# Kernel optimization log

Hardware: AMD Instinct MI355X
Metric: run time of the kernel (lower is better)

## Reference

```python
import jax, jax.numpy as jnp
import numpy as np

N, IN_DIM, OUT_DIM, H = 8192, 128, 128, 2
HD = OUT_DIM // H
NEG_SLOPE = 0.2


def setup_inputs() -> dict:
    key = jax.random.key(0)
    k1, k2, k3, k4, k5 = jax.random.split(key, 5)
    x = jax.random.normal(k1, (N, IN_DIM), dtype=jnp.float32)
    adj = jax.random.randint(k2, (N, N), 0, 2).astype(jnp.float32)
    W = jax.random.normal(k3, (IN_DIM, OUT_DIM), dtype=jnp.float32) / np.sqrt(IN_DIM)
    a_src = jax.random.normal(k4, (H, HD), dtype=jnp.float32) * 0.01
    a_dst = jax.random.normal(k5, (H, HD), dtype=jnp.float32) * 0.01
    return {"x": x, "adj": adj, "W": W, "a_src": a_src, "a_dst": a_dst}


def reference(x, adj, W, a_src, a_dst):
    # h: (N, H, HD)
    h = (x @ W).reshape(N, H, HD)
    # per-node additive score halves: (N, H)
    e_src = jnp.einsum('nhd,hd->nh', h, a_src)
    e_dst = jnp.einsum('nhd,hd->nh', h, a_dst)
    # attn logits: (N_i, N_j, H); torch code adds e_src[i] + e_dst[j]
    logits = jax.nn.leaky_relu(e_src[:, None, :] + e_dst[None, :, :], NEG_SLOPE)
    logits = jnp.where(adj[:, :, None] > 0, logits, -jnp.inf)
    # softmax over neighbor axis j (dim=1), matching F.softmax(attn, dim=1)
    attn = jax.nn.softmax(logits, axis=1)
    # dropout omitted (eval mode)
    out = jnp.einsum('ijh,jhd->ihd', attn, h).reshape(N, OUT_DIM)
    return out
```

## Files before the change

### kernel.cpp

```cpp
#include <hip/hip_runtime.h>
#include <hip/hip_bf16.h>

#define N 8192
#define IND 128
#define OUTD 128
#define JC 8
#define JLEN 1024
#define OSTEPS 8
#define NW64 (N / 64)

typedef float f32x4 __attribute__((ext_vector_type(4)));
typedef short s16x8 __attribute__((ext_vector_type(8)));
typedef _Float16 f16;
typedef _Float16 f16x4 __attribute__((ext_vector_type(4)));

static __device__ inline unsigned short f2bf(float f) {
    union { float f; unsigned u; } v; v.f = f;
    unsigned u = v.u + 0x7fffu + ((v.u >> 16) & 1u);
    return (unsigned short)(u >> 16);
}
static __device__ inline float bf2f(unsigned short b) {
    union { unsigned u; float f; } v; v.u = ((unsigned)b) << 16;
    return v.f;
}
static __device__ __forceinline__ unsigned pkbf(float a, float b) {
    __hip_bfloat162 t = __float22bfloat162_rn(make_float2(a, b));
    unsigned u;
    __builtin_memcpy(&u, &t, 4);
    return u;
}

__global__ __launch_bounds__(256) void k0_pack(const float* __restrict__ adj,
                                               unsigned long long* __restrict__ bits) {
    const int row = blockIdx.x;
    const int wave = threadIdx.x >> 6, lane = threadIdx.x & 63;
    const float* src = adj + (size_t)row * N + wave * 2048;
    unsigned long long acc = 0;
#pragma unroll 8
    for (int t = 0; t < 32; ++t) {
        float v = src[t * 64 + lane];
        unsigned long long b = __ballot(v != 0.0f);
        if (lane == t) acc = b;
    }
    if (lane < 32)
        bits[(size_t)row * NW64 + wave * 32 + lane] = acc;
}

__global__ __launch_bounds__(256) void k1_xw(const float* __restrict__ x,
                                             const float* __restrict__ W,
                                             unsigned short* __restrict__ hT) {
    __shared__ unsigned short Wl[128 * 130];
    const int tid = threadIdx.x;
    {
        int k = tid >> 1, n0 = (tid & 1) * 64;
        const float4* src = (const float4*)(W + k * 128 + n0);
#pragma unroll
        for (int v = 0; v < 16; ++v) {
            float4 f = src[v];
            int base = k * 130 + n0 + v * 4;
            Wl[base + 0] = f2bf(f.x);
            Wl[base + 1] = f2bf(f.y);
            Wl[base + 2] = f2bf(f.z);
            Wl[base + 3] = f2bf(f.w);
        }
    }
    __syncthreads();
    const int wave = tid >> 6, lane = tid & 63;
    const int m = lane & 15, quad = lane >> 4;
    const int ibase = blockIdx.x * 64 + wave * 16;
    const int irow = ibase + m;

    f32x4 acc[8];
#pragma unroll
    for (int t = 0; t < 8; ++t) acc[t] = (f32x4){0.f, 0.f, 0.f, 0.f};

#pragma unroll
    for (int ks = 0; ks < 4; ++ks) {
        const int k0 = ks * 32 + quad * 8;
        const float4* xp = (const float4*)(x + (size_t)irow * 128 + k0);
        float4 xa = xp[0], xb = xp[1];
        s16x8 afrag;
        afrag[0] = (short)f2bf(xa.x); afrag[1] = (short)f2bf(xa.y);
        afrag[2] = (short)f2bf(xa.z); afrag[3] = (short)f2bf(xa.w);
        afrag[4] = (short)f2bf(xb.x); afrag[5] = (short)f2bf(xb.y);
        afrag[6] = (short)f2bf(xb.z); afrag[7] = (short)f2bf(xb.w);
#pragma unroll
        for (int nt = 0; nt < 8; ++nt) {
            const int n = nt * 16 + m;
            s16x8 bfrag;
#pragma unroll
            for (int j = 0; j < 8; ++j)
                bfrag[j] = (short)Wl[(k0 + j) * 130 + n];
            acc[nt] = __builtin_amdgcn_mfma_f32_16x16x32_bf16(afrag, bfrag, acc[nt], 0, 0, 0);
        }
    }
#pragma unroll
    for (int nt = 0; nt < 8; ++nt) {
        const int c = nt * 16 + m;
        const int i0 = ibase + quad * 4;
        ushort4 pk;
        pk.x = f2bf(acc[nt][0]); pk.y = f2bf(acc[nt][1]);
        pk.z = f2bf(acc[nt][2]); pk.w = f2bf(acc[nt][3]);
        *(ushort4*)(hT + (size_t)c * N + i0) = pk;
    }
}

__global__ __launch_bounds__(256) void k2_e(const unsigned short* __restrict__ hT,
                                            const float* __restrict__ a_src,
                                            const float* __restrict__ a_dst,
                                            float* __restrict__ As, float* __restrict__ Cs,
                                            float4* __restrict__ BD) {
    const int i = blockIdx.x * 256 + threadIdx.x;
    float es0 = 0.f, ed0 = 0.f, es1 = 0.f, ed1 = 0.f;
#pragma unroll 8
    for (int c = 0; c < 128; ++c) {
        float v = bf2f(hT[(size_t)c * N + i]);
        float as = a_src[c], ad = a_dst[c];
        if (c < 64) { es0 += v * as; ed0 += v * ad; }
        else        { es1 += v * as; ed1 += v * ad; }
    }
    As[i]     = __expf(es0);
    As[N + i] = __expf(es1);
    Cs[i]     = __expf(0.2f * es0);
    Cs[N + i] = __expf(0.2f * es1);
    float4 bd;
    bd.x = __expf(ed0); bd.y = __expf(0.2f * ed0);
    bd.z = __expf(ed1); bd.w = __expf(0.2f * ed1);
    BD[i] = bd;
}

__global__ __launch_bounds__(256, 4) void k3_main(const unsigned long long* __restrict__ bits,
                                                  const unsigned short* __restrict__ hT,
                                                  const float* __restrict__ As,
                                                  const float* __restrict__ Cs,
                                                  const float4* __restrict__ BD,
                                                  f16* __restrict__ Up,
                                                  float* __restrict__ Lp) {
    __shared__ float4 BDl[JLEN + JLEN / 8];
    const int tid = threadIdx.x;
    const int wave = tid >> 6, lane = tid & 63;
    const int m = lane & 15, quad = lane >> 4;
    const int ibase = blockIdx.x * 64 + wave * 16;
    const int irow = ibase + m;
    const int jc = blockIdx.y;
    const int j0 = jc * JLEN;

    for (int t = tid; t < JLEN; t += 256) BDl[t + (t >> 3)] = BD[j0 + t];

    const float A0 = As[irow], C0 = Cs[irow];
    const float A1 = As[N + irow], C1 = Cs[N + irow];

    f32x4 acc[2][4];
#pragma unroll
    for (int h = 0; h < 2; ++h)
#pragma unroll
        for (int nt = 0; nt < 4; ++nt) acc[h][nt] = (f32x4){0.f, 0.f, 0.f, 0.f};
    f32x4 accS[2];
    accS[0] = (f32x4){0.f, 0.f, 0.f, 0.f};
    accS[1] = (f32x4){0.f, 0.f, 0.f, 0.f};

    s16x8 ones;
#pragma unroll
    for (int t = 0; t < 8; ++t) ones[t] = (short)0x3F80;

    const unsigned long long* mrow = bits + (size_t)irow * NW64 + (j0 >> 6);
    const int shbase = quad * 8;
    __syncthreads();

#pragma unroll 2
    for (int os = 0; os < OSTEPS; ++os) {
        const unsigned long long mk0 = mrow[os * 2];
        const unsigned long long mk1 = mrow[os * 2 + 1];
#pragma unroll
        for (int kc = 0; kc < 4; ++kc) {
            const int jq = j0 + os * 128 + kc * 32 + quad * 8;
            s16x8 h0[4], h1[4];
#pragma unroll
            for (int nt = 0; nt < 4; ++nt) {
                h0[nt] = *(const s16x8*)(hT + (size_t)(nt * 16 + m) * N + jq);
                h1[nt] = *(const s16x8*)(hT + (size_t)(nt * 16 + m + 64) * N + jq);
            }
            const unsigned long long mk = (kc < 2) ? mk0 : mk1;
            const unsigned mbyte = (unsigned)(mk >> ((kc & 1) * 32 + shbase)) & 0xffu;

            const int bb = os * 128 + kc * 32 + quad * 8;
            const int bidx = bb + (bb >> 3);
            float pv0[8], pv1[8];
#pragma unroll
            for (int jj = 0; jj < 8; ++jj) {
                float4 bd = BDl[bidx + jj];
                float w0 = fmaxf(A0 * bd.x, C0 * bd.y);
                float w1 = fmaxf(A1 * bd.z, C1 * bd.w);
                bool on = (mbyte >> jj) & 1u;
                pv0[jj] = on ? w0 : 0.0f;
                pv1[jj] = on ? w1 : 0.0f;
            }
            unsigned pu0[4], pu1[4];
#pragma unroll
            for (int t = 0; t < 4; ++t) {
                pu0[t] = pkbf(pv0[t * 2], pv0[t * 2 + 1]);
                pu1[t] = pkbf(pv1[t * 2], pv1[t * 2 + 1]);
            }
            s16x8 p0, p1;
            __builtin_memcpy(&p0, pu0, 16);
            __builtin_memcpy(&p1, pu1, 16);

#pragma unroll
            for (int nt = 0; nt < 4; ++nt) {
                acc[0][nt] = __builtin_amdgcn_mfma_f32_16x16x32_bf16(p0, h0[nt], acc[0][nt], 0, 0, 0);
                acc[1][nt] = __builtin_amdgcn_mfma_f32_16x16x32_bf16(p1, h1[nt], acc[1][nt], 0, 0, 0);
            }
            accS[0] = __builtin_amdgcn_mfma_f32_16x16x32_bf16(p0, ones, accS[0], 0, 0, 0);
            accS[1] = __builtin_amdgcn_mfma_f32_16x16x32_bf16(p1, ones, accS[1], 0, 0, 0);
        }
    }

    f16* Ub = Up + (size_t)jc * N * 128;
#pragma unroll
    for (int h = 0; h < 2; ++h)
#pragma unroll
        for (int nt = 0; nt < 4; ++nt) {
            const int c = h * 64 + nt * 16 + m;
            const int ib = ibase + quad * 4;
#pragma unroll
            for (int r = 0; r < 4; ++r)
                Ub[(size_t)(ib + r) * 128 + c] = (f16)acc[h][nt][r];
        }
    if (m == 0) {
#pragma unroll
        for (int h = 0; h < 2; ++h)
#pragma unroll
            for (int r = 0; r < 4; ++r)
                Lp[((size_t)jc * 2 + h) * N + ibase + quad * 4 + r] = accS[h][r];
    }
}

__global__ __launch_bounds__(256) void k4_reduce(const f16* __restrict__ Up,
                                                 const float* __restrict__ Lp,
                                                 float* __restrict__ out) {
    const int base = (blockIdx.x * 256 + threadIdx.x) * 4;
    const int i = base >> 7, c = base & 127, h = c >> 6;
    float su0 = 0.f, su1 = 0.f, su2 = 0.f, su3 = 0.f, sl = 0.f;
#pragma unroll
    for (int jcc = 0; jcc < JC; ++jcc) {
        f16x4 u = *(const f16x4*)(Up + (size_t)jcc * N * 128 + base);
        su0 += (float)u[0]; su1 += (float)u[1];
        su2 += (float)u[2]; su3 += (float)u[3];
        sl += Lp[((size_t)jcc * 2 + h) * N + i];
    }
    float inv = 1.0f / sl;
    float4 o; o.x = su0 * inv; o.y = su1 * inv; o.z = su2 * inv; o.w = su3 * inv;
    *(float4*)(out + base) = o;
}

extern "C" void kernel_launch(void* const* d_in, const int* in_sizes, int n_in,
                              void* d_out, int out_size, void* d_ws, size_t ws_size,
                              hipStream_t stream) {
    const float* x     = (const float*)d_in[0];
    const float* adj   = (const float*)d_in[1];
    const float* W     = (const float*)d_in[2];
    const float* a_src = (const float*)d_in[3];
    const float* a_dst = (const float*)d_in[4];
    float* out = (float*)d_out;
    char* ws = (char*)d_ws;

    size_t off = 0;
    unsigned short* hT = (unsigned short*)(ws + off); off += (size_t)128 * N * 2;
    float* As = (float*)(ws + off); off += (size_t)2 * N * 4;
    float* Cs = (float*)(ws + off); off += (size_t)2 * N * 4;
    float4* BD = (float4*)(ws + off); off += (size_t)N * 16;
    unsigned long long* bits = (unsigned long long*)(ws + off); off += (size_t)N * NW64 * 8;

    f16* Up = (f16*)(ws + off);
    float* Lp = (float*)(ws + off + (size_t)JC * N * 128 * 2);

    k0_pack<<<N, 256, 0, stream>>>(adj, bits);
    k1_xw<<<N / 64, 256, 0, stream>>>(x, W, hT);
    k2_e<<<N / 256, 256, 0, stream>>>(hT, a_src, a_dst, As, Cs, BD);
    dim3 g3(N / 64, JC);
    k3_main<<<g3, 256, 0, stream>>>(bits, hT, As, Cs, BD, Up, Lp);
    k4_reduce<<<(N * 128) / (256 * 4), 256, 0, stream>>>(Up, Lp, out);
}
```

Before: 515.0 us.

## Double-buffer hT loads in main loop and reduce split-K partials with atomics

```diff
diff --git a/kernel.cpp b/kernel.cpp
--- a/kernel.cpp
+++ b/kernel.cpp
@@ -6,13 +6,11 @@
 #define OUTD 128
 #define JC 8
 #define JLEN 1024
-#define OSTEPS 8
+#define TSTEPS 32
 #define NW64 (N / 64)
 
 typedef float f32x4 __attribute__((ext_vector_type(4)));
 typedef short s16x8 __attribute__((ext_vector_type(8)));
-typedef _Float16 f16;
-typedef _Float16 f16x4 __attribute__((ext_vector_type(4)));
 
 static __device__ inline unsigned short f2bf(float f) {
     union { float f; unsigned u; } v; v.f = f;
@@ -36,7 +34,7 @@
     const int wave = threadIdx.x >> 6, lane = threadIdx.x & 63;
     const float* src = adj + (size_t)row * N + wave * 2048;
     unsigned long long acc = 0;
-#pragma unroll 8
+#pragma unroll
     for (int t = 0; t < 32; ++t) {
         float v = src[t * 64 + lane];
         unsigned long long b = __ballot(v != 0.0f);
@@ -129,14 +127,15 @@
     BD[i] = bd;
 }
 
-__global__ __launch_bounds__(256, 4) void k3_main(const unsigned long long* __restrict__ bits,
+__global__ __launch_bounds__(256, 3) void k3_main(const unsigned long long* __restrict__ bits,
                                                   const unsigned short* __restrict__ hT,
                                                   const float* __restrict__ As,
                                                   const float* __restrict__ Cs,
                                                   const float4* __restrict__ BD,
-                                                  f16* __restrict__ Up,
+                                                  float* __restrict__ Up,
                                                   float* __restrict__ Lp) {
-    __shared__ float4 BDl[JLEN + JLEN / 8];
+    __shared__ float smem[4 * 16 * 129];
+    float4* BDl = (float4*)smem;
     const int tid = threadIdx.x;
     const int wave = tid >> 6, lane = tid & 63;
     const int m = lane & 15, quad = lane >> 4;
@@ -164,92 +163,99 @@
     for (int t = 0; t < 8; ++t) ones[t] = (short)0x3F80;
 
     const unsigned long long* mrow = bits + (size_t)irow * NW64 + (j0 >> 6);
-    const int shbase = quad * 8;
     __syncthreads();
 
-#pragma unroll 2
-    for (int os = 0; os < OSTEPS; ++os) {
-        const unsigned long long mk0 = mrow[os * 2];
-        const unsigned long long mk1 = mrow[os * 2 + 1];
-#pragma unroll
-        for (int kc = 0; kc < 4; ++kc) {
-            const int jq = j0 + os * 128 + kc * 32 + quad * 8;
-            s16x8 h0[4], h1[4];
-#pragma unroll
-            for (int nt = 0; nt < 4; ++nt) {
-                h0[nt] = *(const s16x8*)(hT + (size_t)(nt * 16 + m) * N + jq);
-                h1[nt] = *(const s16x8*)(hT + (size_t)(nt * 16 + m + 64) * N + jq);
-            }
-            const unsigned long long mk = (kc < 2) ? mk0 : mk1;
-            const unsigned mbyte = (unsigned)(mk >> ((kc & 1) * 32 + shbase)) & 0xffu;
-
-            const int bb = os * 128 + kc * 32 + quad * 8;
-            const int bidx = bb + (bb >> 3);
-            float pv0[8], pv1[8];
-#pragma unroll
-            for (int jj = 0; jj < 8; ++jj) {
-                float4 bd = BDl[bidx + jj];
-                float w0 = fmaxf(A0 * bd.x, C0 * bd.y);
-                float w1 = fmaxf(A1 * bd.z, C1 * bd.w);
-                bool on = (mbyte >> jj) & 1u;
-                pv0[jj] = on ? w0 : 0.0f;
-                pv1[jj] = on ? w1 : 0.0f;
-            }
-            unsigned pu0[4], pu1[4];
-#pragma unroll
-            for (int t = 0; t < 4; ++t) {
-                pu0[t] = pkbf(pv0[t * 2], pv0[t * 2 + 1]);
-                pu1[t] = pkbf(pv1[t * 2], pv1[t * 2 + 1]);
-            }
-            s16x8 p0, p1;
-            __builtin_memcpy(&p0, pu0, 16);
-            __builtin_memcpy(&p1, pu1, 16);
-
-#pragma unroll
-            for (int nt = 0; nt < 4; ++nt) {
-                acc[0][nt] = __builtin_amdgcn_mfma_f32_16x16x32_bf16(p0, h0[nt], acc[0][nt], 0, 0, 0);
-                acc[1][nt] = __builtin_amdgcn_mfma_f32_16x16x32_bf16(p1, h1[nt], acc[1][nt], 0, 0, 0);
-            }
-            accS[0] = __builtin_amdgcn_mfma_f32_16x16x32_bf16(p0, ones, accS[0], 0, 0, 0);
-            accS[1] = __builtin_amdgcn_mfma_f32_16x16x32_bf16(p1, ones, accS[1], 0, 0, 0);
-        }
-    }
-
-    f16* Ub = Up + (size_t)jc * N * 128;
+    s16x8 hb[2][8];
+    {
+        const int jq0 = j0 + quad * 8;
+#pragma unroll
+        for (int nt = 0; nt < 4; ++nt) {
+            hb[0][nt]     = *(const s16x8*)(hT + (size_t)(nt * 16 + m) * N + jq0);
+            hb[0][4 + nt] = *(const s16x8*)(hT + (size_t)(nt * 16 + m + 64) * N + jq0);
+        }
+    }
+
+#pragma unroll 4
+    for (int t = 0; t < TSTEPS; ++t) {
+        const int cur = t & 1, nxt = cur ^ 1;
+        const int tn = (t < TSTEPS - 1) ? t + 1 : t;
+        const int jqn = j0 + tn * 32 + quad * 8;
+#pragma unroll
+        for (int nt = 0; nt < 4; ++nt) {
+            hb[nxt][nt]     = *(const s16x8*)(hT + (size_t)(nt * 16 + m) * N + jqn);
+            hb[nxt][4 + nt] = *(const s16x8*)(hT + (size_t)(nt * 16 + m + 64) * N + jqn);
+        }
+
+        const unsigned long long mk = mrow[t >> 1];
+        const unsigned mbyte = (unsigned)(mk >> ((t & 1) * 32 + quad * 8)) & 0xffu;
+
+        const int bb = t * 32 + quad * 8;
+        const int bidx = bb + (bb >> 3);
+        float pv0[8], pv1[8];
+#pragma unroll
+        for (int jj = 0; jj < 8; ++jj) {
+            float4 bd = BDl[bidx + jj];
+            float w0 = fmaxf(A0 * bd.x, C0 * bd.y);
+            float w1 = fmaxf(A1 * bd.z, C1 * bd.w);
+            bool on = (mbyte >> jj) & 1u;
+            pv0[jj] = on ? w0 : 0.0f;
+            pv1[jj] = on ? w1 : 0.0f;
+        }
+        unsigned pu0[4], pu1[4];
+#pragma unroll
+        for (int q = 0; q < 4; ++q) {
+            pu0[q] = pkbf(pv0[q * 2], pv0[q * 2 + 1]);
+            pu1[q] = pkbf(pv1[q * 2], pv1[q * 2 + 1]);
+        }
+        s16x8 p0, p1;
+        __builtin_memcpy(&p0, pu0, 16);
+        __builtin_memcpy(&p1, pu1, 16);
+
+#pragma unroll
+        for (int nt = 0; nt < 4; ++nt) {
+            acc[0][nt] = __builtin_amdgcn_mfma_f32_16x16x32_bf16(p0, hb[cur][nt], acc[0][nt], 0, 0, 0);
+            acc[1][nt] = __builtin_amdgcn_mfma_f32_16x16x32_bf16(p1, hb[cur][4 + nt], acc[1][nt], 0, 0, 0);
+        }
+        accS[0] = __builtin_amdgcn_mfma_f32_16x16x32_bf16(p0, ones, accS[0], 0, 0, 0);
+        accS[1] = __builtin_amdgcn_mfma_f32_16x16x32_bf16(p1, ones, accS[1], 0, 0, 0);
+    }
+
+    __syncthreads();
+    float* sm = smem + wave * 16 * 129;
 #pragma unroll
     for (int h = 0; h < 2; ++h)
 #pragma unroll
         for (int nt = 0; nt < 4; ++nt) {
             const int c = h * 64 + nt * 16 + m;
-            const int ib = ibase + quad * 4;
 #pragma unroll
             for (int r = 0; r < 4; ++r)
-                Ub[(size_t)(ib + r) * 128 + c] = (f16)acc[h][nt][r];
-        }
+                sm[(quad * 4 + r) * 129 + c] = acc[h][nt][r];
+        }
+#pragma unroll
+    for (int r16 = 0; r16 < 16; ++r16) {
+        float v0 = sm[r16 * 129 + lane];
+        float v1 = sm[r16 * 129 + 64 + lane];
+        const size_t o = (size_t)(ibase + r16) * 128 + lane;
+        atomicAdd(&Up[o], v0);
+        atomicAdd(&Up[o + 64], v1);
+    }
     if (m == 0) {
 #pragma unroll
         for (int h = 0; h < 2; ++h)
 #pragma unroll
             for (int r = 0; r < 4; ++r)
-                Lp[((size_t)jc * 2 + h) * N + ibase + quad * 4 + r] = accS[h][r];
-    }
-}
-
-__global__ __launch_bounds__(256) void k4_reduce(const f16* __restrict__ Up,
-                                                 const float* __restrict__ Lp,
-                                                 float* __restrict__ out) {
+                atomicAdd(&Lp[h * N + ibase + quad * 4 + r], accS[h][r]);
+    }
+}
+
+__global__ __launch_bounds__(256) void k4_norm(const float* __restrict__ Up,
+                                               const float* __restrict__ Lp,
+                                               float* __restrict__ out) {
     const int base = (blockIdx.x * 256 + threadIdx.x) * 4;
-    const int i = base >> 7, c = base & 127, h = c >> 6;
-    float su0 = 0.f, su1 = 0.f, su2 = 0.f, su3 = 0.f, sl = 0.f;
-#pragma unroll
-    for (int jcc = 0; jcc < JC; ++jcc) {
-        f16x4 u = *(const f16x4*)(Up + (size_t)jcc * N * 128 + base);
-        su0 += (float)u[0]; su1 += (float)u[1];
-        su2 += (float)u[2]; su3 += (float)u[3];
-        sl += Lp[((size_t)jcc * 2 + h) * N + i];
-    }
-    float inv = 1.0f / sl;
-    float4 o; o.x = su0 * inv; o.y = su1 * inv; o.z = su2 * inv; o.w = su3 * inv;
+    const int i = base >> 7, h = (base & 127) >> 6;
+    float4 u = *(const float4*)(Up + base);
+    float inv = 1.0f / Lp[h * N + i];
+    float4 o; o.x = u.x * inv; o.y = u.y * inv; o.z = u.z * inv; o.w = u.w * inv;
     *(float4*)(out + base) = o;
 }
 
@@ -270,14 +276,15 @@
     float* Cs = (float*)(ws + off); off += (size_t)2 * N * 4;
     float4* BD = (float4*)(ws + off); off += (size_t)N * 16;
     unsigned long long* bits = (unsigned long long*)(ws + off); off += (size_t)N * NW64 * 8;
-
-    f16* Up = (f16*)(ws + off);
-    float* Lp = (float*)(ws + off + (size_t)JC * N * 128 * 2);
+    float* Up = (float*)(ws + off); off += (size_t)N * 128 * 4;
+    float* Lp = (float*)(ws + off); off += (size_t)2 * N * 4;
+
+    hipMemsetAsync(Up, 0, (size_t)N * 128 * 4 + (size_t)2 * N * 4, stream);
 
     k0_pack<<<N, 256, 0, stream>>>(adj, bits);
     k1_xw<<<N / 64, 256, 0, stream>>>(x, W, hT);
     k2_e<<<N / 256, 256, 0, stream>>>(hT, a_src, a_dst, As, Cs, BD);
     dim3 g3(N / 64, JC);
     k3_main<<<g3, 256, 0, stream>>>(bits, hT, As, Cs, BD, Up, Lp);
-    k4_reduce<<<(N * 128) / (256 * 4), 256, 0, stream>>>(Up, Lp, out);
-}
+    k4_norm<<<(N * 128) / (256 * 4), 256, 0, stream>>>(Up, Lp, out);
+}
```

After: 541.3 us. 5.1% more time.

## Stage hT tiles in LDS via async loads, pack BD to bf16, coalesce output

Applied to the files above, without the earlier changes.

```diff
diff --git a/kernel.cpp b/kernel.cpp
--- a/kernel.cpp
+++ b/kernel.cpp
@@ -6,13 +6,18 @@
 #define OUTD 128
 #define JC 8
 #define JLEN 1024
-#define OSTEPS 8
+#define SUBC 8
+#define SUBJ 128
+#define TSUB 4
 #define NW64 (N / 64)
 
 typedef float f32x4 __attribute__((ext_vector_type(4)));
 typedef short s16x8 __attribute__((ext_vector_type(8)));
 typedef _Float16 f16;
+typedef _Float16 f16x2 __attribute__((ext_vector_type(2)));
 typedef _Float16 f16x4 __attribute__((ext_vector_type(4)));
+typedef long long ll2 __attribute__((ext_vector_type(2)));
+typedef unsigned int u32x4 __attribute__((ext_vector_type(4)));
 
 static __device__ inline unsigned short f2bf(float f) {
     union { float f; unsigned u; } v; v.f = f;
@@ -28,6 +33,11 @@
     unsigned u;
     __builtin_memcpy(&u, &t, 4);
     return u;
+}
+static __device__ __forceinline__ void async16(const void* g, void* l) {
+    __builtin_amdgcn_global_load_lds(
+        (const __attribute__((address_space(1))) unsigned int*)g,
+        (__attribute__((address_space(3))) unsigned int*)l, 16, 0, 0);
 }
 
 __global__ __launch_bounds__(256) void k0_pack(const float* __restrict__ adj,
@@ -36,7 +46,7 @@
     const int wave = threadIdx.x >> 6, lane = threadIdx.x & 63;
     const float* src = adj + (size_t)row * N + wave * 2048;
     unsigned long long acc = 0;
-#pragma unroll 8
+#pragma unroll
     for (int t = 0; t < 32; ++t) {
         float v = src[t * 64 + lane];
         unsigned long long b = __ballot(v != 0.0f);
@@ -109,7 +119,7 @@
                                             const float* __restrict__ a_src,
                                             const float* __restrict__ a_dst,
                                             float* __restrict__ As, float* __restrict__ Cs,
-                                            float4* __restrict__ BD) {
+                                            uint2* __restrict__ BDh) {
     const int i = blockIdx.x * 256 + threadIdx.x;
     float es0 = 0.f, ed0 = 0.f, es1 = 0.f, ed1 = 0.f;
 #pragma unroll 8
@@ -123,20 +133,22 @@
     As[N + i] = __expf(es1);
     Cs[i]     = __expf(0.2f * es0);
     Cs[N + i] = __expf(0.2f * es1);
-    float4 bd;
-    bd.x = __expf(ed0); bd.y = __expf(0.2f * ed0);
-    bd.z = __expf(ed1); bd.w = __expf(0.2f * ed1);
-    BD[i] = bd;
+    uint2 bd;
+    bd.x = pkbf(__expf(ed0), __expf(0.2f * ed0));
+    bd.y = pkbf(__expf(ed1), __expf(0.2f * ed1));
+    BDh[i] = bd;
 }
 
 __global__ __launch_bounds__(256, 4) void k3_main(const unsigned long long* __restrict__ bits,
-                                                  const unsigned short* __restrict__ hT,
+                                                  const unsigned short* __restrict__ hTg,
                                                   const float* __restrict__ As,
                                                   const float* __restrict__ Cs,
-                                                  const float4* __restrict__ BD,
+                                                  const uint2* __restrict__ BDh,
                                                   f16* __restrict__ Up,
                                                   float* __restrict__ Lp) {
-    __shared__ float4 BDl[JLEN + JLEN / 8];
+    __shared__ float4 smem4[2112];
+    unsigned short* hTl = (unsigned short*)smem4;
+    uint2* bdl = (uint2*)((char*)smem4 + 32768);
     const int tid = threadIdx.x;
     const int wave = tid >> 6, lane = tid & 63;
     const int m = lane & 15, quad = lane >> 4;
@@ -145,8 +157,6 @@
     const int jc = blockIdx.y;
     const int j0 = jc * JLEN;
 
-    for (int t = tid; t < JLEN; t += 256) BDl[t + (t >> 3)] = BD[j0 + t];
-
     const float A0 = As[irow], C0 = Cs[irow];
     const float A1 = As[N + irow], C1 = Cs[N + irow];
 
@@ -163,43 +173,64 @@
 #pragma unroll
     for (int t = 0; t < 8; ++t) ones[t] = (short)0x3F80;
 
-    const unsigned long long* mrow = bits + (size_t)irow * NW64 + (j0 >> 6);
-    const int shbase = quad * 8;
-    __syncthreads();
-
-#pragma unroll 2
-    for (int os = 0; os < OSTEPS; ++os) {
-        const unsigned long long mk0 = mrow[os * 2];
-        const unsigned long long mk1 = mrow[os * 2 + 1];
-#pragma unroll
-        for (int kc = 0; kc < 4; ++kc) {
-            const int jq = j0 + os * 128 + kc * 32 + quad * 8;
+    const int crow = lane >> 4;
+    const int gd = lane & 15;
+
+#pragma unroll 1
+    for (int sc = 0; sc < SUBC; ++sc) {
+        const int jb = j0 + sc * SUBJ;
+        if (sc) __syncthreads();
+        ll2 mk = *(const ll2*)(bits + (size_t)irow * NW64 + (jb >> 6));
+        if (wave == 0)
+            async16(BDh + jb + lane * 2, bdl);
+#pragma unroll
+        for (int rr = 0; rr < 8; ++rr) {
+            const int rg = wave * 8 + rr;
+            const int c = rg * 4 + crow;
+            const int gs = gd ^ (c & 7);
+            async16(hTg + (size_t)c * N + jb + gs * 8, hTl + rg * 512);
+        }
+        __syncthreads();
+
+#pragma unroll
+        for (int t = 0; t < TSUB; ++t) {
+            u32x4 bq[4];
+            const u32x4* bp = (const u32x4*)(bdl + (t * 32 + quad * 8));
+#pragma unroll
+            for (int z = 0; z < 4; ++z) bq[z] = bp[z];
             s16x8 h0[4], h1[4];
+            const int gr = t * 4 + quad;
 #pragma unroll
             for (int nt = 0; nt < 4; ++nt) {
-                h0[nt] = *(const s16x8*)(hT + (size_t)(nt * 16 + m) * N + jq);
-                h1[nt] = *(const s16x8*)(hT + (size_t)(nt * 16 + m + 64) * N + jq);
+                const int c0 = nt * 16 + m;
+                const int go = (gr ^ (c0 & 7)) * 8;
+                h0[nt] = *(const s16x8*)(hTl + c0 * 128 + go);
+                h1[nt] = *(const s16x8*)(hTl + (c0 + 64) * 128 + go);
             }
-            const unsigned long long mk = (kc < 2) ? mk0 : mk1;
-            const unsigned mbyte = (unsigned)(mk >> ((kc & 1) * 32 + shbase)) & 0xffu;
-
-            const int bb = os * 128 + kc * 32 + quad * 8;
-            const int bidx = bb + (bb >> 3);
+            const unsigned long long mw =
+                (t < 2) ? (unsigned long long)mk[0] : (unsigned long long)mk[1];
+            const unsigned mbyte = (unsigned)(mw >> ((t & 1) * 32 + quad * 8)) & 0xffu;
+
             float pv0[8], pv1[8];
 #pragma unroll
             for (int jj = 0; jj < 8; ++jj) {
-                float4 bd = BDl[bidx + jj];
-                float w0 = fmaxf(A0 * bd.x, C0 * bd.y);
-                float w1 = fmaxf(A1 * bd.z, C1 * bd.w);
+                const unsigned p0u = bq[jj >> 1][(jj & 1) * 2];
+                const unsigned p1u = bq[jj >> 1][(jj & 1) * 2 + 1];
+                float B0 = __uint_as_float(p0u << 16);
+                float D0 = __uint_as_float(p0u & 0xffff0000u);
+                float B1 = __uint_as_float(p1u << 16);
+                float D1 = __uint_as_float(p1u & 0xffff0000u);
+                float w0 = fmaxf(A0 * B0, C0 * D0);
+                float w1 = fmaxf(A1 * B1, C1 * D1);
                 bool on = (mbyte >> jj) & 1u;
                 pv0[jj] = on ? w0 : 0.0f;
                 pv1[jj] = on ? w1 : 0.0f;
             }
             unsigned pu0[4], pu1[4];
 #pragma unroll
-            for (int t = 0; t < 4; ++t) {
-                pu0[t] = pkbf(pv0[t * 2], pv0[t * 2 + 1]);
-                pu1[t] = pkbf(pv1[t * 2], pv1[t * 2 + 1]);
+            for (int q = 0; q < 4; ++q) {
+                pu0[q] = pkbf(pv0[q * 2], pv0[q * 2 + 1]);
+                pu1[q] = pkbf(pv1[q * 2], pv1[q * 2 + 1]);
             }
             s16x8 p0, p1;
             __builtin_memcpy(&p0, pu0, 16);
@@ -215,17 +246,25 @@
         }
     }
 
-    f16* Ub = Up + (size_t)jc * N * 128;
+    __syncthreads();
+    float* smf = (float*)smem4 + wave * (16 * 129);
 #pragma unroll
     for (int h = 0; h < 2; ++h)
 #pragma unroll
         for (int nt = 0; nt < 4; ++nt) {
             const int c = h * 64 + nt * 16 + m;
-            const int ib = ibase + quad * 4;
 #pragma unroll
             for (int r = 0; r < 4; ++r)
-                Ub[(size_t)(ib + r) * 128 + c] = (f16)acc[h][nt][r];
-        }
+                smf[(quad * 4 + r) * 129 + c] = acc[h][nt][r];
+        }
+    f16* Ub = Up + (size_t)jc * N * 128;
+#pragma unroll
+    for (int r16 = 0; r16 < 16; ++r16) {
+        float v0 = smf[r16 * 129 + lane * 2];
+        float v1 = smf[r16 * 129 + lane * 2 + 1];
+        f16x2 pk; pk[0] = (f16)v0; pk[1] = (f16)v1;
+        *(f16x2*)(Ub + (size_t)(ibase + r16) * 128 + lane * 2) = pk;
+    }
     if (m == 0) {
 #pragma unroll
         for (int h = 0; h < 2; ++h)
@@ -268,16 +307,15 @@
     unsigned short* hT = (unsigned short*)(ws + off); off += (size_t)128 * N * 2;
     float* As = (float*)(ws + off); off += (size_t)2 * N * 4;
     float* Cs = (float*)(ws + off); off += (size_t)2 * N * 4;
-    float4* BD = (float4*)(ws + off); off += (size_t)N * 16;
+    uint2* BDh = (uint2*)(ws + off); off += (size_t)N * 8;
     unsigned long long* bits = (unsigned long long*)(ws + off); off += (size_t)N * NW64 * 8;
-
-    f16* Up = (f16*)(ws + off);
-    float* Lp = (float*)(ws + off + (size_t)JC * N * 128 * 2);
+    f16* Up = (f16*)(ws + off); off += (size_t)JC * N * 128 * 2;
+    float* Lp = (float*)(ws + off); off += (size_t)JC * 2 * N * 4;
 
     k0_pack<<<N, 256, 0, stream>>>(adj, bits);
     k1_xw<<<N / 64, 256, 0, stream>>>(x, W, hT);
-    k2_e<<<N / 256, 256, 0, stream>>>(hT, a_src, a_dst, As, Cs, BD);
+    k2_e<<<N / 256, 256, 0, stream>>>(hT, a_src, a_dst, As, Cs, BDh);
     dim3 g3(N / 64, JC);
-    k3_main<<<g3, 256, 0, stream>>>(bits, hT, As, Cs, BD, Up, Lp);
+    k3_main<<<g3, 256, 0, stream>>>(bits, hT, As, Cs, BDh, Up, Lp);
     k4_reduce<<<(N * 128) / (256 * 4), 256, 0, stream>>>(Up, Lp, out);
 }
```

New measurement: 436.2 us (median of 2 runs). 1.18x faster.
